# Performance work log

Measured on AMD Instinct MI355X. Metric: run time of the kernel, lower is better.

## Reference

```python
import jax, jax.numpy as jnp
import numpy as np

T, IN, OUT, M, C = 8192, 1024, 1024, 128, 32
MIN_PERIOD, MAX_PERIOD = 1.0, 1024.0
LN_EPS = 1e-5


def _linear_params(key, in_f, out_f):
    # equinox nn.Linear default init: U(-1/sqrt(in), 1/sqrt(in)) for weight and bias
    lim = 1.0 / np.sqrt(in_f)
    kw, kb = jax.random.split(key)
    w = jax.random.uniform(kw, (out_f, in_f), minval=-lim, maxval=lim, dtype=jnp.float32)
    b = jax.random.uniform(kb, (out_f,), minval=-lim, maxval=lim, dtype=jnp.float32)
    return w, b


def setup_inputs() -> dict:
    key = jax.random.key(0)
    ks = jax.random.split(key, 8)
    x = jax.random.normal(ks[0], (T, IN), dtype=jnp.float32)
    done = jax.random.bernoulli(ks[1], 0.01, (T,))  # sparse episode resets
    state_re = jnp.zeros((1, M, C), jnp.float32)
    state_im = jnp.zeros((1, M, C), jnp.float32)
    # ffa.init(memory_size, context_size): decay rates a and context frequencies b
    a = jnp.linspace(1e-6, 0.5, M, dtype=jnp.float32)
    b = 2.0 * jnp.pi / jnp.linspace(MIN_PERIOD, MAX_PERIOD, C, dtype=jnp.float32)
    pre_w, pre_b = _linear_params(ks[2], IN, M)
    gin_w, gin_b = _linear_params(ks[3], IN, M)
    gout_w, gout_b = _linear_params(ks[4], IN, OUT)
    skip_w, skip_b = _linear_params(ks[5], IN, OUT)
    mix_w, mix_b = _linear_params(ks[6], 2 * M * C, OUT)
    return dict(x=x, done=done, state_re=state_re, state_im=state_im, a=a, b=b,
                pre_w=pre_w, pre_b=pre_b, gin_w=gin_w, gin_b=gin_b,
                gout_w=gout_w, gout_b=gout_b, skip_w=skip_w, skip_b=skip_b,
                mix_w=mix_w, mix_b=mix_b)


def _ffm_forward(x, done, s0, a, b, pre_w, pre_b, gin_w, gin_b,
                 gout_w, gout_b, skip_w, skip_b, mix_w, mix_b):
    # input gating: gated_x[t, m]
    gate_in = jax.nn.sigmoid(x @ gin_w.T + gin_b)            # [T, M]
    gated_x = (x @ pre_w.T + pre_b) * gate_in                # [T, M]

    # gamma[m, c] = exp(-|a_m| + i b_c): per-step complex decay/rotation
    re, im = jnp.broadcast_arrays(-jnp.abs(a)[:, None], b[None, :])
    gamma = jnp.exp(jax.lax.complex(re, im))                 # [M, C] complex64

    def step(s, inp):
        # s_t = gamma * s_{t-1} * (1 - done_t) + x_t 1^T  (reset before accumulate)
        xt, dt = inp
        keep = jnp.where(dt, 0.0, 1.0).astype(jnp.float32)
        s = keep * s * gamma + xt[:, None]
        return s, s

    _, states = jax.lax.scan(step, s0, (gated_x.astype(jnp.complex64), done))  # [T, M, C]

    # mix: concat(real, imag) along last axis -> [T, M, 2C] -> [T, 2MC]
    z_in = jnp.concatenate([states.real, states.imag], axis=-1).reshape(states.shape[0], -1)
    z = z_in @ mix_w.T + mix_b                               # [T, OUT]

    gate_out = jax.nn.sigmoid(x @ gout_w.T + gout_b)         # [T, OUT]
    skip = x @ skip_w.T + skip_b                             # [T, OUT]

    # LayerNorm without weight/bias (eps = 1e-5)
    zg = z * gate_out
    mu = zg.mean(-1, keepdims=True)
    var = ((zg - mu) ** 2).mean(-1, keepdims=True)
    ln = (zg - mu) / jnp.sqrt(var + LN_EPS)

    out = ln + skip * (1.0 - gate_out)
    return out, states


def reference(x, done, state_re, state_im, a, b, pre_w, pre_b, gin_w, gin_b,
              gout_w, gout_b, skip_w, skip_b, mix_w, mix_b):
    s0 = jax.lax.complex(state_re, state_im)[0]              # [M, C]
    return _ffm_forward(x, done, s0, a, b, pre_w, pre_b, gin_w, gin_b,
                        gout_w, gout_b, skip_w, skip_b, mix_w, mix_b)
```

## Files before the change

kernel.cpp:

```cpp
#include <hip/hip_runtime.h>
#include <stdint.h>

#define T_DIM 8192
#define IN_DIM 1024
#define OUT_DIM 1024
#define M_DIM 128
#define SEG 64
#define NSEG (T_DIM / SEG)
#define CHUNK 2048
#define KS_FB 4

typedef __bf16 bf16x8 __attribute__((ext_vector_type(8)));
typedef float f32x4 __attribute__((ext_vector_type(4)));

__device__ inline unsigned short f2bf(float f) {
  unsigned int u = __float_as_uint(f);
  unsigned int r = (u + 0x7fffu + ((u >> 16) & 1u)) >> 16;
  return (unsigned short)r;
}
__device__ inline float bf2f(unsigned short h) {
  return __uint_as_float(((unsigned int)h) << 16);
}
__device__ inline float sigm(float v) { return 1.f / (1.f + expf(-v)); }

__global__ __launch_bounds__(256) void f2bf_kernel(const float* __restrict__ in,
                                                   unsigned short* __restrict__ out, long n) {
  long i = (long)blockIdx.x * 256 + threadIdx.x;
  if (i < n) out[i] = f2bf(in[i]);
}

__global__ __launch_bounds__(256) void permconv_kernel(const float* __restrict__ w,
                                                       unsigned short* __restrict__ o, long n) {
  long i = (long)blockIdx.x * 256 + threadIdx.x;
  if (i >= n) return;
  long row = i >> 13;
  int k = (int)(i & 8191);
  int src = ((k >> 6) << 6) | ((k & 1) << 5) | ((k >> 1) & 31);
  o[i] = f2bf(w[(row << 13) + src]);
}

__global__ __launch_bounds__(256) void wcat_kernel(const float* __restrict__ gout_w,
                                                   const float* __restrict__ skip_w,
                                                   const float* __restrict__ pre_w,
                                                   const float* __restrict__ gin_w,
                                                   unsigned short* __restrict__ o) {
  long i = (long)blockIdx.x * 256 + threadIdx.x;
  if (i >= (long)2304 * 1024) return;
  int row = (int)(i >> 10), col = (int)(i & 1023);
  float v;
  if (row < 1024)       v = gout_w[row * 1024 + col];
  else if (row < 2048)  v = skip_w[(row - 1024) * 1024 + col];
  else if (row < 2176)  v = pre_w[(row - 2048) * 1024 + col];
  else                  v = gin_w[(row - 2176) * 1024 + col];
  o[i] = f2bf(v);
}

__global__ void bcat_kernel(const float* __restrict__ gout_b, const float* __restrict__ skip_b,
                            const float* __restrict__ pre_b, const float* __restrict__ gin_b,
                            float* __restrict__ dst) {
  int i = blockIdx.x * 256 + threadIdx.x;
  if (i >= 2304) return;
  float v;
  if (i < 1024)      v = gout_b[i];
  else if (i < 2048) v = skip_b[i - 1024];
  else if (i < 2176) v = pre_b[i - 2048];
  else               v = gin_b[i - 2176];
  dst[i] = v;
}

__global__ void gamma_kernel(const float* __restrict__ a, const float* __restrict__ b,
                             float2* __restrict__ gam, float2* __restrict__ gamL) {
  int tid = blockIdx.x * 256 + threadIdx.x;
  int m = tid >> 5, c = tid & 31;
  double aa = fabs((double)a[m]);
  double ang = (double)b[c];
  double mag = exp(-aa);
  gam[tid] = make_float2((float)(mag * cos(ang)), (float)(mag * sin(ang)));
  double magL = exp(-aa * (double)SEG);
  double angL = ang * (double)SEG;
  gamL[tid] = make_float2((float)(magL * cos(angL)), (float)(magL * sin(angL)));
}

#define GEMM_KLOOP(AP, BP, LDK)                                                        \
  for (int k0 = 0; k0 < kloop_end; k0 += 64) {                                         \
    _Pragma("unroll")                                                                  \
    for (int cc = 0; cc < 4; ++cc) {                                                   \
      __builtin_amdgcn_global_load_lds(                                                \
          (const __attribute__((address_space(1))) void*)(AP + k0 + (size_t)cc * 32 * (LDK)), \
          (__attribute__((address_space(3))) void*)(As + cc * 2048 + w * 512), 16, 0, 0);     \
      __builtin_amdgcn_global_load_lds(                                                \
          (const __attribute__((address_space(1))) void*)(BP + k0 + (size_t)cc * 32 * (LDK)), \
          (__attribute__((address_space(3))) void*)(Bs + cc * 2048 + w * 512), 16, 0, 0);     \
    }                                                                                  \
    __syncthreads();                                                                   \
    _Pragma("unroll")                                                                  \
    for (int kk = 0; kk < 2; ++kk) {                                                   \
      const int eb = kk ? e1 : e0;                                                     \
      const char* Bp = (const char*)Bpbase + eb;                                       \
      bf16x8 b0 = *(const bf16x8*)(Bp);                                                \
      bf16x8 b1 = *(const bf16x8*)(Bp + 2048);                                         \
      bf16x8 b2 = *(const bf16x8*)(Bp + 4096);                                         \
      bf16x8 b3 = *(const bf16x8*)(Bp + 6144);                                         \
      const char* Ap = (const char*)Apbase + eb;                                       \
      _Pragma("unroll")                                                                \
      for (int i = 0; i < 4; ++i) {                                                    \
        bf16x8 af = *(const bf16x8*)(Ap + i * 2048);                                   \
        acc[i][0] = __builtin_amdgcn_mfma_f32_16x16x32_bf16(af, b0, acc[i][0], 0, 0, 0);\
        acc[i][1] = __builtin_amdgcn_mfma_f32_16x16x32_bf16(af, b1, acc[i][1], 0, 0, 0);\
        acc[i][2] = __builtin_amdgcn_mfma_f32_16x16x32_bf16(af, b2, acc[i][2], 0, 0, 0);\
        acc[i][3] = __builtin_amdgcn_mfma_f32_16x16x32_bf16(af, b3, acc[i][3], 0, 0, 0);\
      }                                                                                \
    }                                                                                  \
    __syncthreads();                                                                   \
  }

#define GEMM_PREAMBLE                                                                  \
  const int tid = threadIdx.x;                                                         \
  const int lane = tid & 63, w = tid >> 6;                                             \
  const int wr = w >> 1, wc = w & 1;                                                   \
  f32x4 acc[4][4] = {};                                                                \
  const int srow = tid >> 3;                                                           \
  const int ksw = ((tid & 7) ^ (srow & 7)) * 8;                                        \
  const int l15 = lane & 15;                                                           \
  const int krd = (lane >> 4) * 8;                                                     \
  const int rsw = (lane & 7) << 3;                                                     \
  const int e0 = (krd ^ rsw) * 2;                                                      \
  const int e1 = ((32 + krd) ^ rsw) * 2;                                               \
  const unsigned short* Apbase = &As[(wr * 64 + l15) * 64];                            \
  const unsigned short* Bpbase = &Bs[(wc * 64 + l15) * 64];

__global__ __launch_bounds__(256, 4) void gemm_gs_kernel(
    const unsigned short* __restrict__ A, const unsigned short* __restrict__ B,
    const float* __restrict__ bias, unsigned short* __restrict__ gs,
    float* __restrict__ tmp) {
  __shared__ __align__(16) unsigned short As[128 * 64];
  __shared__ __align__(16) unsigned short Bs[128 * 64];
  const int xcd = blockIdx.x & 7;
  const int idx = blockIdx.x >> 3;
  const int bn = idx % 18;
  const int bm = xcd * 8 + idx / 18;
  const int n0 = bn * 128, t0 = bm * 128;
  GEMM_PREAMBLE
  const unsigned short* Ab = A + (size_t)(t0 + srow) * 1024 + ksw;
  const unsigned short* Bb = B + (size_t)(n0 + srow) * 1024 + ksw;
  const int kloop_end = 1024;
  GEMM_KLOOP(Ab, Bb, 1024)

  const int rbase = t0 + wr * 64 + ((lane >> 4) * 4);
  const int cbase = n0 + wc * 64 + l15;
#pragma unroll
  for (int j = 0; j < 4; ++j) {
    const int col = cbase + j * 16;
    const float bv = bias[col];
#pragma unroll
    for (int i = 0; i < 4; ++i) {
#pragma unroll
      for (int r = 0; r < 4; ++r) {
        float v = acc[i][j][r] + bv;
        int row = rbase + i * 16 + r;
        if (col < 2048) gs[(size_t)row * 2048 + col] = f2bf(v);
        else            tmp[(size_t)row * 256 + (col - 2048)] = v;
      }
    }
  }
}

__global__ __launch_bounds__(512, 2) void gemm_mix256_kernel(
    const unsigned short* __restrict__ A, const unsigned short* __restrict__ B,
    float* __restrict__ partials) {
  __shared__ __align__(16) unsigned short As[2][256 * 64];
  __shared__ __align__(16) unsigned short Bs[2][256 * 64];
  const int xcd = blockIdx.x & 7;
  const int idx = blockIdx.x >> 3;
  const int ks = xcd >> 2;
  const int bm = (xcd & 3) * 8 + (idx >> 2);
  const int bn = idx & 3;
  const int t0 = bm * 256, n0 = bn * 256;
  const int tid = threadIdx.x;
  const int lane = tid & 63;
  const int w8 = tid >> 6;
  const int wr = w8 >> 2;
  const int wcol = w8 & 3;

  f32x4 acc[8][4] = {};

  const int srow = tid >> 3;
  const int ksw = ((tid & 7) ^ (srow & 7)) * 8;
  const unsigned short* Ab = A + (size_t)(t0 + srow) * 8192 + ks * 4096 + ksw;
  const unsigned short* Bb = B + (size_t)(n0 + srow) * 8192 + ks * 4096 + ksw;

  const int l15 = lane & 15;
  const int krd = (lane >> 4) * 8;
  const int rsw = (lane & 7) << 3;
  const int e0 = (krd ^ rsw) * 2;
  const int e1 = ((32 + krd) ^ rsw) * 2;

#define STAGE256(buf, k0c)                                                              \
  {                                                                                     \
    _Pragma("unroll")                                                                   \
    for (int j = 0; j < 4; ++j)                                                         \
      __builtin_amdgcn_global_load_lds(                                                 \
          (const __attribute__((address_space(1))) void*)(Ab + (k0c) + (size_t)j * 64 * 8192), \
          (__attribute__((address_space(3))) void*)(&As[buf][j * 4096 + tid * 8]), 16, 0, 0);  \
    _Pragma("unroll")                                                                   \
    for (int j = 0; j < 4; ++j)                                                         \
      __builtin_amdgcn_global_load_lds(                                                 \
          (const __attribute__((address_space(1))) void*)(Bb + (k0c) + (size_t)j * 64 * 8192), \
          (__attribute__((address_space(3))) void*)(&Bs[buf][j * 4096 + tid * 8]), 16, 0, 0);  \
  }

  const int iters = 4096 / 64;
  STAGE256(0, 0)
  int cur = 0;

  for (int t = 0; t < iters; ++t) {
    __builtin_amdgcn_s_barrier();
    __builtin_amdgcn_sched_barrier(0);
    const int k1 = (t + 1 < iters) ? (t + 1) * 64 : t * 64;
    if (cur) { STAGE256(0, k1) } else { STAGE256(1, k1) }
    __builtin_amdgcn_sched_barrier(0);
    asm volatile("s_waitcnt vmcnt(8)" ::: "memory");
    __builtin_amdgcn_sched_barrier(0);
    __builtin_amdgcn_s_barrier();
    __builtin_amdgcn_sched_barrier(0);

    const unsigned short* Apb = &As[cur][(wr * 128 + l15) * 64];
    const unsigned short* Bpb = &Bs[cur][(wcol * 64 + l15) * 64];
#pragma unroll
    for (int s = 0; s < 2; ++s) {
      const int eb = s ? e1 : e0;
      bf16x8 bf0 = *(const bf16x8*)((const char*)Bpb + eb);
      bf16x8 bf1 = *(const bf16x8*)((const char*)Bpb + 2048 + eb);
      bf16x8 bf2 = *(const bf16x8*)((const char*)Bpb + 4096 + eb);
      bf16x8 bf3 = *(const bf16x8*)((const char*)Bpb + 6144 + eb);
      __builtin_amdgcn_s_setprio(1);
#pragma unroll
      for (int i = 0; i < 8; ++i) {
        bf16x8 af = *(const bf16x8*)((const char*)Apb + i * 2048 + eb);
        acc[i][0] = __builtin_amdgcn_mfma_f32_16x16x32_bf16(af, bf0, acc[i][0], 0, 0, 0);
        acc[i][1] = __builtin_amdgcn_mfma_f32_16x16x32_bf16(af, bf1, acc[i][1], 0, 0, 0);
        acc[i][2] = __builtin_amdgcn_mfma_f32_16x16x32_bf16(af, bf2, acc[i][2], 0, 0, 0);
        acc[i][3] = __builtin_amdgcn_mfma_f32_16x16x32_bf16(af, bf3, acc[i][3], 0, 0, 0);
      }
      __builtin_amdgcn_s_setprio(0);
    }
    cur ^= 1;
  }

  float* Cp = partials + (size_t)ks * T_DIM * 1024;
  const int rbase = t0 + wr * 128 + ((lane >> 4) * 4);
  const int cbase = n0 + wcol * 64 + l15;
#pragma unroll
  for (int j = 0; j < 4; ++j) {
    const int col = cbase + j * 16;
#pragma unroll
    for (int i = 0; i < 8; ++i)
#pragma unroll
      for (int r = 0; r < 4; ++r)
        Cp[(size_t)(rbase + i * 16 + r) * 1024 + col] = acc[i][j][r];
  }
#undef STAGE256
}

__global__ __launch_bounds__(256, 4) void gemm_splitk_kernel(
    const unsigned short* __restrict__ A, const unsigned short* __restrict__ B,
    float* __restrict__ partials, int nbm, int kslice, int prows) {
  __shared__ __align__(16) unsigned short As[128 * 64];
  __shared__ __align__(16) unsigned short Bs[128 * 64];
  const int cpx = gridDim.x >> 3;
  const int wid = (blockIdx.x & 7) * cpx + (blockIdx.x >> 3);
  const int bm = wid % nbm;
  const int bn = (wid / nbm) & 7;
  const int ks = wid / (nbm * 8);
  const int n0 = bn * 128, t0 = bm * 128;
  GEMM_PREAMBLE
  const unsigned short* Ab = A + (size_t)(t0 + srow) * 8192 + ks * kslice + ksw;
  const unsigned short* Bb = B + (size_t)(n0 + srow) * 8192 + ks * kslice + ksw;
  const int kloop_end = kslice;
  GEMM_KLOOP(Ab, Bb, 8192)

  float* Cp = partials + (size_t)ks * prows * 1024;
  const int rbase = t0 + wr * 64 + ((lane >> 4) * 4);
  const int cbase = n0 + wc * 64 + l15;
#pragma unroll
  for (int j = 0; j < 4; ++j) {
    const int col = cbase + j * 16;
#pragma unroll
    for (int i = 0; i < 4; ++i)
#pragma unroll
      for (int r = 0; r < 4; ++r)
        Cp[(size_t)(rbase + i * 16 + r) * 1024 + col] = acc[i][j][r];
  }
}

__global__ __launch_bounds__(256) void reduce_kernel(const f32x4* __restrict__ partials,
                                                     const f32x4* __restrict__ bias4,
                                                     f32x4* __restrict__ outc) {
  int i = blockIdx.x * 256 + threadIdx.x;
  const size_t stride = (size_t)CHUNK * 256;
  f32x4 s = partials[i];
#pragma unroll
  for (int p = 1; p < KS_FB; ++p) s += partials[(size_t)p * stride + i];
  s += bias4[i & 255];
  outc[i] = s;
}

__global__ __launch_bounds__(256) void gated_kernel(const float* __restrict__ tmp,
                                                    float* __restrict__ gated) {
  int i = blockIdx.x * 256 + threadIdx.x;
  int t = i >> 7, m = i & 127;
  float p = tmp[t * 256 + m];
  float g = tmp[t * 256 + 128 + m];
  gated[i] = p * sigm(g);
}

__global__ __launch_bounds__(256) void scan_p1_kernel(
    const float* __restrict__ gated, const int* __restrict__ done,
    const float2* __restrict__ gam, const float2* __restrict__ gamL,
    float2* __restrict__ carryA, float2* __restrict__ carryB) {
  int gid = blockIdx.x * 256 + threadIdx.x;
  int seg = gid >> 12, tid = gid & 4095;
  int m = tid >> 5;
  float2 g = gam[tid];
  int t0 = seg * SEG;
  float sr = 0.f, si = 0.f, keep_all = 1.f;
  for (int tt = 0; tt < SEG; ++tt) {
    int t = t0 + tt;
    float xv = gated[t * M_DIM + m];
    bool d = done[t] != 0;
    float pr = d ? 0.f : sr;
    float pi = d ? 0.f : si;
    if (d) keep_all = 0.f;
    sr = fmaf(g.x, pr, fmaf(-g.y, pi, xv));
    si = fmaf(g.y, pr, g.x * pi);
  }
  carryB[(size_t)seg * 4096 + tid] = make_float2(sr, si);
  float2 gL = gamL[tid];
  carryA[(size_t)seg * 4096 + tid] = make_float2(keep_all * gL.x, keep_all * gL.y);
}

__global__ __launch_bounds__(256) void scan_p2_kernel(
    const float2* __restrict__ carryA, float2* __restrict__ carryB,
    const float* __restrict__ s0_re, const float* __restrict__ s0_im) {
  int tid = blockIdx.x * 256 + threadIdx.x;
  float sr = s0_re[tid], si = s0_im[tid];
  for (int p = 0; p < NSEG; ++p) {
    size_t idx = (size_t)p * 4096 + tid;
    float2 A = carryA[idx];
    float2 B = carryB[idx];
    carryB[idx] = make_float2(sr, si);
    float nr = fmaf(A.x, sr, fmaf(-A.y, si, B.x));
    float ni = fmaf(A.y, sr, fmaf(A.x, si, B.y));
    sr = nr; si = ni;
  }
}

__global__ __launch_bounds__(256) void scan_p3_kernel(
    const float* __restrict__ gated, const int* __restrict__ done,
    const float2* __restrict__ gam, const float2* __restrict__ segstart,
    float* __restrict__ out_states, int pair_mode,
    unsigned int* __restrict__ st_bf, int tbase) {
  int gid = blockIdx.x * 256 + threadIdx.x;
  int segl = gid >> 12, tid = gid & 4095;
  int m = tid >> 5;
  int seg = tbase / SEG + segl;
  float2 g = gam[tid];
  float2 s = segstart[(size_t)seg * 4096 + tid];
  float sr = s.x, si = s.y;
  int t0 = seg * SEG;
  for (int tt = 0; tt < SEG; ++tt) {
    int t = t0 + tt;
    float xv = gated[t * M_DIM + m];
    bool d = done[t] != 0;
    float pr = d ? 0.f : sr;
    float pi = d ? 0.f : si;
    sr = fmaf(g.x, pr, fmaf(-g.y, pi, xv));
    si = fmaf(g.y, pr, g.x * pi);
    if (pair_mode) {
      ((float2*)out_states)[(size_t)t * 4096 + tid] = make_float2(sr, si);
    } else {
      out_states[(size_t)t * 4096 + tid] = sr;
    }
    st_bf[(size_t)(t - tbase) * 4096 + tid] =
        (unsigned int)f2bf(sr) | ((unsigned int)f2bf(si) << 16);
  }
}

__global__ __launch_bounds__(256) void ln_kernel(const float* __restrict__ partials, int nred,
                                                 const float* __restrict__ mixb,
                                                 const unsigned short* __restrict__ gs,
                                                 float* __restrict__ out) {
  const int t = blockIdx.x;
  const int tid = threadIdx.x;
  __shared__ float sm[8];
  const int o = tid * 4;
  f32x4 z;
  if (nred == 0) {
    z = *(const f32x4*)&out[(size_t)t * 1024 + o];
  } else {
    z = *(const f32x4*)&partials[(size_t)t * 1024 + o];
    for (int p = 1; p < nred; ++p)
      z += *(const f32x4*)&partials[(size_t)p * T_DIM * 1024 + (size_t)t * 1024 + o];
    z += *(const f32x4*)&mixb[o];
  }
  ushort4 gu = *(const ushort4*)&gs[(size_t)t * 2048 + o];
  ushort4 su = *(const ushort4*)&gs[(size_t)t * 2048 + 1024 + o];
  float g[4], sk[4], zg[4];
  g[0] = sigm(bf2f(gu.x)); g[1] = sigm(bf2f(gu.y));
  g[2] = sigm(bf2f(gu.z)); g[3] = sigm(bf2f(gu.w));
  sk[0] = bf2f(su.x); sk[1] = bf2f(su.y); sk[2] = bf2f(su.z); sk[3] = bf2f(su.w);
  float sum = 0.f;
#pragma unroll
  for (int j = 0; j < 4; ++j) { zg[j] = z[j] * g[j]; sum += zg[j]; }
#pragma unroll
  for (int off = 32; off > 0; off >>= 1) sum += __shfl_down(sum, off, 64);
  if ((tid & 63) == 0) sm[tid >> 6] = sum;
  __syncthreads();
  const float mu = (sm[0] + sm[1] + sm[2] + sm[3]) * (1.f / 1024.f);
  float sq = 0.f;
#pragma unroll
  for (int j = 0; j < 4; ++j) { float d = zg[j] - mu; sq += d * d; }
#pragma unroll
  for (int off = 32; off > 0; off >>= 1) sq += __shfl_down(sq, off, 64);
  if ((tid & 63) == 0) sm[4 + (tid >> 6)] = sq;
  __syncthreads();
  const float var = (sm[4] + sm[5] + sm[6] + sm[7]) * (1.f / 1024.f);
  const float rstd = 1.f / sqrtf(var + 1e-5f);
  f32x4 res;
#pragma unroll
  for (int j = 0; j < 4; ++j) res[j] = (zg[j] - mu) * rstd + sk[j] * (1.f - g[j]);
  *(f32x4*)&out[(size_t)t * 1024 + o] = res;
}

extern "C" void kernel_launch(void* const* d_in, const int* in_sizes, int n_in,
                              void* d_out, int out_size, void* d_ws, size_t ws_size,
                              hipStream_t stream) {
  const float* x      = (const float*)d_in[0];
  const int*   done   = (const int*)d_in[1];
  const float* s0_re  = (const float*)d_in[2];
  const float* s0_im  = (const float*)d_in[3];
  const float* a      = (const float*)d_in[4];
  const float* b      = (const float*)d_in[5];
  const float* pre_w  = (const float*)d_in[6];
  const float* pre_b  = (const float*)d_in[7];
  const float* gin_w  = (const float*)d_in[8];
  const float* gin_b  = (const float*)d_in[9];
  const float* gout_w = (const float*)d_in[10];
  const float* gout_b = (const float*)d_in[11];
  const float* skip_w = (const float*)d_in[12];
  const float* skip_b = (const float*)d_in[13];
  const float* mix_w  = (const float*)d_in[14];
  const float* mix_b  = (const float*)d_in[15];

  float* out_f = (float*)d_out;
  float* states_f = out_f + (size_t)T_DIM * OUT_DIM;
  const int pair_mode = (out_size >= 75000000) ? 1 : 0;

  char* ws = (char*)d_ws;
  size_t off = 0;
  auto alloc = [&](size_t bytes) {
    void* p = ws + off;
    off = (off + bytes + 255) & ~(size_t)255;
    return p;
  };
  unsigned short* x_bf   = (unsigned short*)alloc((size_t)T_DIM * IN_DIM * 2);
  unsigned short* Bmix   = (unsigned short*)alloc((size_t)OUT_DIM * 8192 * 2);
  unsigned short* Wgs    = (unsigned short*)alloc((size_t)2304 * IN_DIM * 2);
  float* bias_gs         = (float*)alloc(2304 * 4);
  float* tmp_pg          = (float*)alloc((size_t)T_DIM * 256 * 4);
  float* gated           = (float*)alloc((size_t)T_DIM * M_DIM * 4);
  float2* gam            = (float2*)alloc(4096 * 8);
  float2* gamL           = (float2*)alloc(4096 * 8);
  float2* carryA         = (float2*)alloc((size_t)NSEG * 4096 * 8);
  float2* carryB         = (float2*)alloc((size_t)NSEG * 4096 * 8);
  unsigned short* gs_o   = (unsigned short*)alloc((size_t)T_DIM * 2048 * 2);

  size_t need_main = off + (size_t)T_DIM * 8192 * 2 + (size_t)2 * T_DIM * 1024 * 4 + 1024;
  const int full_path = (ws_size == 0 || ws_size >= need_main) ? 1 : 0;

  dim3 blk(256);
  long nx = (long)T_DIM * IN_DIM;
  f2bf_kernel<<<(unsigned)((nx + 255) / 256), blk, 0, stream>>>(x, x_bf, nx);
  permconv_kernel<<<32768, blk, 0, stream>>>(mix_w, Bmix, 8388608L);
  wcat_kernel<<<9216, blk, 0, stream>>>(gout_w, skip_w, pre_w, gin_w, Wgs);
  bcat_kernel<<<9, blk, 0, stream>>>(gout_b, skip_b, pre_b, gin_b, bias_gs);
  gamma_kernel<<<16, blk, 0, stream>>>(a, b, gam, gamL);

  gemm_gs_kernel<<<1152, blk, 0, stream>>>(x_bf, Wgs, bias_gs, gs_o, tmp_pg);
  gated_kernel<<<(T_DIM * M_DIM) / 256, blk, 0, stream>>>(tmp_pg, gated);

  scan_p1_kernel<<<NSEG * 16, blk, 0, stream>>>(gated, done, gam, gamL, carryA, carryB);
  scan_p2_kernel<<<16, blk, 0, stream>>>(carryA, carryB, s0_re, s0_im);

  if (full_path) {
    unsigned short* st_bf = (unsigned short*)alloc((size_t)T_DIM * 8192 * 2);
    float* partials       = (float*)alloc((size_t)2 * T_DIM * 1024 * 4);
    scan_p3_kernel<<<NSEG * 16, blk, 0, stream>>>(gated, done, gam, carryB,
                                                  states_f, pair_mode,
                                                  (unsigned int*)st_bf, 0);
    gemm_mix256_kernel<<<256, dim3(512), 0, stream>>>(st_bf, Bmix, partials);
    ln_kernel<<<T_DIM, blk, 0, stream>>>(partials, 2, mix_b, gs_o, out_f);
  } else {
    unsigned short* st_bf = (unsigned short*)alloc((size_t)CHUNK * 8192 * 2);
    float* partials       = (float*)alloc((size_t)KS_FB * CHUNK * 1024 * 4);
    for (int ch = 0; ch < T_DIM / CHUNK; ++ch) {
      int tbase = ch * CHUNK;
      scan_p3_kernel<<<(CHUNK / SEG) * 16, blk, 0, stream>>>(gated, done, gam, carryB,
                                                             states_f, pair_mode,
                                                             (unsigned int*)st_bf, tbase);
      gemm_splitk_kernel<<<8 * (CHUNK / 128) * KS_FB, blk, 0, stream>>>(
          st_bf, Bmix, partials, CHUNK / 128, 8192 / KS_FB, CHUNK);
      reduce_kernel<<<CHUNK, blk, 0, stream>>>((const f32x4*)partials, (const f32x4*)mix_b,
                                               (f32x4*)(out_f + (size_t)tbase * OUT_DIM));
    }
    ln_kernel<<<T_DIM, blk, 0, stream>>>(nullptr, 0, mix_b, gs_o, out_f);
  }
  (void)n_in; (void)in_sizes;
}
```

Before: 371.4 us.

## Triple-buffer A tiles in mix GEMM and drop one barrier per iteration

The 256x256 mix GEMM now keeps three LDS buffers for A and two for B. A is prefetched two k-steps ahead and B one step ahead, and each iteration uses a single vmcnt wait plus one barrier instead of two barriers. The inner MFMA loop is regrouped to load four A fragments at once before issuing sixteen MFMAs. LDS use rises to the full 160KB and launch bounds drop to one block per CU, which gives up any chance of two resident blocks.

```diff
diff --git a/kernel.cpp b/kernel.cpp
--- a/kernel.cpp
+++ b/kernel.cpp
@@ -165,10 +165,10 @@
   }
 }
 
-__global__ __launch_bounds__(512, 2) void gemm_mix256_kernel(
+__global__ __launch_bounds__(512, 1) void gemm_mix256_kernel(
     const unsigned short* __restrict__ A, const unsigned short* __restrict__ B,
     float* __restrict__ partials) {
-  __shared__ __align__(16) unsigned short As[2][256 * 64];
+  __shared__ __align__(16) unsigned short As[3][256 * 64];
   __shared__ __align__(16) unsigned short Bs[2][256 * 64];
   const int xcd = blockIdx.x & 7;
   const int idx = blockIdx.x >> 3;
@@ -195,37 +195,45 @@
   const int e0 = (krd ^ rsw) * 2;
   const int e1 = ((32 + krd) ^ rsw) * 2;
 
-#define STAGE256(buf, k0c)                                                              \
+#define STAGE_A3(buf, kt)                                                               \
   {                                                                                     \
     _Pragma("unroll")                                                                   \
     for (int j = 0; j < 4; ++j)                                                         \
       __builtin_amdgcn_global_load_lds(                                                 \
-          (const __attribute__((address_space(1))) void*)(Ab + (k0c) + (size_t)j * 64 * 8192), \
-          (__attribute__((address_space(3))) void*)(&As[buf][j * 4096 + tid * 8]), 16, 0, 0);  \
+          (const __attribute__((address_space(1))) void*)(Ab + (kt) + (size_t)j * 64 * 8192), \
+          (__attribute__((address_space(3))) void*)(&As[buf][j * 4096 + tid * 8]), 16, 0, 0); \
+  }
+#define STAGE_B2(buf, kt)                                                               \
+  {                                                                                     \
     _Pragma("unroll")                                                                   \
     for (int j = 0; j < 4; ++j)                                                         \
       __builtin_amdgcn_global_load_lds(                                                 \
-          (const __attribute__((address_space(1))) void*)(Bb + (k0c) + (size_t)j * 64 * 8192), \
-          (__attribute__((address_space(3))) void*)(&Bs[buf][j * 4096 + tid * 8]), 16, 0, 0);  \
+          (const __attribute__((address_space(1))) void*)(Bb + (kt) + (size_t)j * 64 * 8192), \
+          (__attribute__((address_space(3))) void*)(&Bs[buf][j * 4096 + tid * 8]), 16, 0, 0); \
   }
 
   const int iters = 4096 / 64;
-  STAGE256(0, 0)
-  int cur = 0;
+  STAGE_B2(0, 0)
+  STAGE_A3(0, 0)
+  STAGE_A3(1, 64)
 
   for (int t = 0; t < iters; ++t) {
+    asm volatile("s_waitcnt vmcnt(4)" ::: "memory");
     __builtin_amdgcn_s_barrier();
     __builtin_amdgcn_sched_barrier(0);
-    const int k1 = (t + 1 < iters) ? (t + 1) * 64 : t * 64;
-    if (cur) { STAGE256(0, k1) } else { STAGE256(1, k1) }
-    __builtin_amdgcn_sched_barrier(0);
-    asm volatile("s_waitcnt vmcnt(8)" ::: "memory");
-    __builtin_amdgcn_sched_barrier(0);
-    __builtin_amdgcn_s_barrier();
-    __builtin_amdgcn_sched_barrier(0);
-
-    const unsigned short* Apb = &As[cur][(wr * 128 + l15) * 64];
-    const unsigned short* Bpb = &Bs[cur][(wcol * 64 + l15) * 64];
+    const int tb = (t + 1 < iters) ? (t + 1) * 64 : t * 64;
+    const int ta = (t + 2 < iters) ? (t + 2) * 64 : t * 64;
+    {
+      const int bB = (t + 1) & 1;
+      if (bB) { STAGE_B2(1, tb) } else { STAGE_B2(0, tb) }
+      const int bA = (t + 2) % 3;
+      if (bA == 0) { STAGE_A3(0, ta) }
+      else if (bA == 1) { STAGE_A3(1, ta) }
+      else { STAGE_A3(2, ta) }
+    }
+
+    const unsigned short* Apb = &As[t % 3][(wr * 128 + l15) * 64];
+    const unsigned short* Bpb = &Bs[t & 1][(wcol * 64 + l15) * 64];
 #pragma unroll
     for (int s = 0; s < 2; ++s) {
       const int eb = s ? e1 : e0;
@@ -233,18 +241,33 @@
       bf16x8 bf1 = *(const bf16x8*)((const char*)Bpb + 2048 + eb);
       bf16x8 bf2 = *(const bf16x8*)((const char*)Bpb + 4096 + eb);
       bf16x8 bf3 = *(const bf16x8*)((const char*)Bpb + 6144 + eb);
-      __builtin_amdgcn_s_setprio(1);
-#pragma unroll
-      for (int i = 0; i < 8; ++i) {
-        bf16x8 af = *(const bf16x8*)((const char*)Apb + i * 2048 + eb);
-        acc[i][0] = __builtin_amdgcn_mfma_f32_16x16x32_bf16(af, bf0, acc[i][0], 0, 0, 0);
-        acc[i][1] = __builtin_amdgcn_mfma_f32_16x16x32_bf16(af, bf1, acc[i][1], 0, 0, 0);
-        acc[i][2] = __builtin_amdgcn_mfma_f32_16x16x32_bf16(af, bf2, acc[i][2], 0, 0, 0);
-        acc[i][3] = __builtin_amdgcn_mfma_f32_16x16x32_bf16(af, bf3, acc[i][3], 0, 0, 0);
+#pragma unroll
+      for (int ih = 0; ih < 2; ++ih) {
+        const char* Ap = (const char*)Apb + ih * 8192;
+        bf16x8 a0 = *(const bf16x8*)(Ap + eb);
+        bf16x8 a1 = *(const bf16x8*)(Ap + 2048 + eb);
+        bf16x8 a2 = *(const bf16x8*)(Ap + 4096 + eb);
+        bf16x8 a3 = *(const bf16x8*)(Ap + 6144 + eb);
+        __builtin_amdgcn_s_setprio(1);
+        acc[ih*4+0][0] = __builtin_amdgcn_mfma_f32_16x16x32_bf16(a0, bf0, acc[ih*4+0][0], 0, 0, 0);
+        acc[ih*4+0][1] = __builtin_amdgcn_mfma_f32_16x16x32_bf16(a0, bf1, acc[ih*4+0][1], 0, 0, 0);
+        acc[ih*4+0][2] = __builtin_amdgcn_mfma_f32_16x16x32_bf16(a0, bf2, acc[ih*4+0][2], 0, 0, 0);
+        acc[ih*4+0][3] = __builtin_amdgcn_mfma_f32_16x16x32_bf16(a0, bf3, acc[ih*4+0][3], 0, 0, 0);
+        acc[ih*4+1][0] = __builtin_amdgcn_mfma_f32_16x16x32_bf16(a1, bf0, acc[ih*4+1][0], 0, 0, 0);
+        acc[ih*4+1][1] = __builtin_amdgcn_mfma_f32_16x16x32_bf16(a1, bf1, acc[ih*4+1][1], 0, 0, 0);
+        acc[ih*4+1][2] = __builtin_amdgcn_mfma_f32_16x16x32_bf16(a1, bf2, acc[ih*4+1][2], 0, 0, 0);
+        acc[ih*4+1][3] = __builtin_amdgcn_mfma_f32_16x16x32_bf16(a1, bf3, acc[ih*4+1][3], 0, 0, 0);
+        acc[ih*4+2][0] = __builtin_amdgcn_mfma_f32_16x16x32_bf16(a2, bf0, acc[ih*4+2][0], 0, 0, 0);
+        acc[ih*4+2][1] = __builtin_amdgcn_mfma_f32_16x16x32_bf16(a2, bf1, acc[ih*4+2][1], 0, 0, 0);
+        acc[ih*4+2][2] = __builtin_amdgcn_mfma_f32_16x16x32_bf16(a2, bf2, acc[ih*4+2][2], 0, 0, 0);
+        acc[ih*4+2][3] = __builtin_amdgcn_mfma_f32_16x16x32_bf16(a2, bf3, acc[ih*4+2][3], 0, 0, 0);
+        acc[ih*4+3][0] = __builtin_amdgcn_mfma_f32_16x16x32_bf16(a3, bf0, acc[ih*4+3][0], 0, 0, 0);
+        acc[ih*4+3][1] = __builtin_amdgcn_mfma_f32_16x16x32_bf16(a3, bf1, acc[ih*4+3][1], 0, 0, 0);
+        acc[ih*4+3][2] = __builtin_amdgcn_mfma_f32_16x16x32_bf16(a3, bf2, acc[ih*4+3][2], 0, 0, 0);
+        acc[ih*4+3][3] = __builtin_amdgcn_mfma_f32_16x16x32_bf16(a3, bf3, acc[ih*4+3][3], 0, 0, 0);
+        __builtin_amdgcn_s_setprio(0);
       }
-      __builtin_amdgcn_s_setprio(0);
     }
-    cur ^= 1;
   }
 
   float* Cp = partials + (size_t)ks * T_DIM * 1024;
@@ -259,7 +282,8 @@
       for (int r = 0; r < 4; ++r)
         Cp[(size_t)(rbase + i * 16 + r) * 1024 + col] = acc[i][j][r];
   }
-#undef STAGE256
+#undef STAGE_A3
+#undef STAGE_B2
 }
 
 __global__ __launch_bounds__(256, 4) void gemm_splitk_kernel(
```

Measured after the change: 366.0 us. No clear change (-1.4%).
